# Optimization experiments

Hardware: AMD Instinct MI355X
Metric: run time of the kernel (lower is better)

## Reference

```python
import jax, jax.numpy as jnp
from jax import lax
import numpy as np

L, B, C, H, W = 2, 4, 256, 128, 128
D = C // 2            # complex feature dim per head (embed_dim // 2)
NH = 2                # hardcoded n_heads in ComplexTransformerEncoderLayer
KS, STRIDE, PAD = 9, 8, 4
SCALE = 32.0 ** -0.5  # n_head_channels ** -0.5 (hardcoded 32)

_PNAMES = ['wq','bq','wk','bk','wv','bv','off_dw_w','off_dw_b','off_ln_g','off_ln_b',
           'off_pw_w','fc1_wr','fc1_wi','fc1_br','fc1_bi','fc2_wr','fc2_wi','fc2_br',
           'fc2_bi','ln_grr','ln_gri','ln_gii','ln_br','ln_bi','rpe_table']


def _bilinear(img, grid):
    # img: (Cc, Hi, Wi); grid: (..., 2) with (x, y) in [-1, 1]
    # matches F.grid_sample(mode='bilinear', align_corners=True, padding_mode='zeros')
    Cc, Hi, Wi = img.shape
    x = (grid[..., 0] + 1.0) * 0.5 * (Wi - 1)
    y = (grid[..., 1] + 1.0) * 0.5 * (Hi - 1)
    x0 = jnp.floor(x); y0 = jnp.floor(y)
    x1 = x0 + 1.0; y1 = y0 + 1.0
    wx1 = x - x0; wx0 = 1.0 - wx1
    wy1 = y - y0; wy0 = 1.0 - wy1

    def tap(yy, xx, wgt):
        valid = (xx >= 0) & (xx <= Wi - 1) & (yy >= 0) & (yy <= Hi - 1)
        xi = jnp.clip(xx, 0, Wi - 1).astype(jnp.int32)
        yi = jnp.clip(yy, 0, Hi - 1).astype(jnp.int32)
        v = img[:, yi, xi]                      # (Cc, *grid_shape)
        return v * (wgt * valid.astype(img.dtype))[None]

    return (tap(y0, x0, wy0 * wx0) + tap(y0, x1, wy0 * wx1)
            + tap(y1, x0, wy1 * wx0) + tap(y1, x1, wy1 * wx1))

_grid_sample = jax.vmap(_bilinear)


def _cln(a, b, gam, eps=1e-20):
    # complex layer-norm via 2x2 covariance whitening over the last (feature) dim
    grr, gri, gii, br, bi = gam
    a = a - a.mean(-1, keepdims=True)
    b = b - b.mean(-1, keepdims=True)
    vrr = (a * a).mean(-1, keepdims=True) + eps
    vii = (b * b).mean(-1, keepdims=True) + eps
    vri = (a * b).mean(-1, keepdims=True)
    s = jnp.sqrt(vrr * vii - vri * vri)
    t = jnp.sqrt(vrr + vii + 2.0 * s)
    inv = 1.0 / (s * t)
    wrr = (vii + s) * inv; wii = (vrr + s) * inv; wri = -vri * inv
    na = wrr * a + wri * b
    nb = wri * a + wii * b
    return grr * na + gri * nb + br, gri * na + gii * nb + bi


def _layer(xa, xb, p):
    res_a = xa.reshape(B * NH, D, H * W).transpose(2, 0, 1)  # (HW, B*NH, D)
    res_b = xb.reshape(B * NH, D, H * W).transpose(2, 0, 1)

    def proj(x, w, bias):  # 1x1 conv
        return jnp.einsum('bchw,oc->bohw', x, w) + bias[None, :, None, None]

    qa = proj(xa, p['wq'], p['bq'])
    qb = proj(xb, p['wq'], p['bq'])

    def conv_offset(q):
        y = lax.conv_general_dilated(q, p['off_dw_w'], (STRIDE, STRIDE),
                                     ((PAD, PAD), (PAD, PAD)),
                                     feature_group_count=C,
                                     dimension_numbers=('NCHW', 'OIHW', 'NCHW'))
        y = y + p['off_dw_b'][None, :, None, None]
        m = y.mean(1, keepdims=True)
        v = ((y - m) ** 2).mean(1, keepdims=True)
        y = (y - m) * lax.rsqrt(v + 1e-5)
        y = y * p['off_ln_g'][None, :, None, None] + p['off_ln_b'][None, :, None, None]
        y = jax.nn.gelu(y, approximate=False)
        return jnp.einsum('bchw,pc->bhwp', y, p['off_pw_w'])  # (B, Hk, Wk, 2) in (y, x)

    off_a = conv_offset(qa)
    off_b = conv_offset(qb)
    Hk, Wk = off_a.shape[1], off_a.shape[2]
    ns = Hk * Wk

    ry = jnp.linspace(0.5, Hk - 0.5, Hk) / (Hk - 1.0) * 2.0 - 1.0
    rx = jnp.linspace(0.5, Wk - 0.5, Wk) / (Wk - 1.0) * 2.0 - 1.0
    ref = jnp.stack(jnp.meshgrid(ry, rx, indexing='ij'), -1)  # (Hk, Wk, 2) (y, x)
    pos_a = off_a + ref
    pos_b = off_b + ref

    xs_a = _grid_sample(xa, pos_a[..., ::-1])  # (B, C, Hk, Wk)
    xs_b = _grid_sample(xb, pos_b[..., ::-1])

    ka = proj(xs_a, p['wk'], p['bk']).reshape(B * NH, D, ns)
    va = proj(xs_a, p['wv'], p['bv']).reshape(B * NH, D, ns)
    kb = proj(xs_b, p['wk'], p['bk']).reshape(B * NH, D, ns)
    vb = proj(xs_b, p['wv'], p['bv']).reshape(B * NH, D, ns)
    qa_ = qa.reshape(B * NH, D, H * W)
    qb_ = qb.reshape(B * NH, D, H * W)

    # Re( q * conj(k) ); imaginary part is discarded by attn.real in the original
    attn = SCALE * (jnp.einsum('bcm,bcn->bmn', qa_, ka)
                    + jnp.einsum('bcm,bcn->bmn', qb_, kb))

    # deformable RPE bias; only the real (a) branch survives attn.real
    gy = jnp.arange(H, dtype=xa.dtype) / (H - 1.0) * 2.0 - 1.0
    gx = jnp.arange(W, dtype=xa.dtype) / (W - 1.0) * 2.0 - 1.0
    qg = jnp.stack(jnp.meshgrid(gy, gx, indexing='ij'), -1).reshape(H * W, 2)
    disp_a = (qg[None, :, None, :] - pos_a.reshape(B, ns, 2)[:, None, :, :]) * 0.5
    rpe = jnp.broadcast_to(p['rpe_table'][None], (B, NH, 2 * H - 1, 2 * W - 1))
    bias_a = _grid_sample(rpe, disp_a[..., ::-1]).reshape(B * NH, H * W, ns)

    attn = jax.nn.softmax(attn + bias_a, axis=2)
    oa = jnp.einsum('bmn,bcn->bcm', attn, va).transpose(2, 0, 1)  # (HW, B*NH, D)
    ob = jnp.einsum('bmn,bcn->bcm', attn, vb).transpose(2, 0, 1)

    oa, ob = _cln(oa, ob, (p['ln_grr'][0], p['ln_gri'][0], p['ln_gii'][0],
                           p['ln_br'][0], p['ln_bi'][0]))
    xa2 = res_a + oa
    xb2 = res_b + ob

    def clinear(a, b, wr, wi, br, bi):
        ya = a @ wr.T - b @ wi.T + br
        yb = a @ wi.T + b @ wr.T + bi
        return ya, yb

    ha, hb = clinear(xa2, xb2, p['fc1_wr'], p['fc1_wi'], p['fc1_br'], p['fc1_bi'])
    ha = jax.nn.relu(ha); hb = jax.nn.relu(hb)
    ha, hb = clinear(ha, hb, p['fc2_wr'], p['fc2_wi'], p['fc2_br'], p['fc2_bi'])
    ha, hb = _cln(ha, hb, (p['ln_grr'][1], p['ln_gri'][1], p['ln_gii'][1],
                           p['ln_br'][1], p['ln_bi'][1]))
    xa3 = xa2 + ha
    xb3 = xb2 + hb
    return (xa3.transpose(1, 2, 0).reshape(B, C, H, W),
            xb3.transpose(1, 2, 0).reshape(B, C, H, W))


def _forward(x_A, x_B, stacked):
    for l in range(L):
        p = {n: stacked[n][l] for n in _PNAMES}
        x_A, x_B = _layer(x_A, x_B, p)
    return x_A, x_B


def setup_inputs():
    key = jax.random.key(0)
    ks = jax.random.split(key, 12)
    f32 = jnp.float32
    return {
        'x_A': jax.random.normal(ks[0], (B, C, H, W), f32),
        'x_B': jax.random.normal(ks[1], (B, C, H, W), f32),
        'wq': jax.random.normal(ks[2], (L, C, C), f32) / np.float32(np.sqrt(C)),
        'bq': jnp.zeros((L, C), f32),
        'wk': jax.random.normal(ks[3], (L, C, C), f32) / np.float32(np.sqrt(C)),
        'bk': jnp.zeros((L, C), f32),
        'wv': jax.random.normal(ks[4], (L, C, C), f32) / np.float32(np.sqrt(C)),
        'bv': jnp.zeros((L, C), f32),
        'off_dw_w': jax.random.normal(ks[5], (L, C, 1, KS, KS), f32) * 0.05,
        'off_dw_b': jnp.zeros((L, C), f32),
        'off_ln_g': jnp.ones((L, C), f32),
        'off_ln_b': jnp.zeros((L, C), f32),
        'off_pw_w': jax.random.normal(ks[6], (L, 2, C), f32) * 0.01,
        'fc1_wr': jax.random.normal(ks[7], (L, D, D), f32) / np.float32(np.sqrt(D)),
        'fc1_wi': jax.random.normal(ks[8], (L, D, D), f32) / np.float32(np.sqrt(D)),
        'fc1_br': jnp.zeros((L, D), f32),
        'fc1_bi': jnp.zeros((L, D), f32),
        'fc2_wr': jax.random.normal(ks[9], (L, D, D), f32) / np.float32(np.sqrt(D)),
        'fc2_wi': jax.random.normal(ks[10], (L, D, D), f32) / np.float32(np.sqrt(D)),
        'fc2_br': jnp.zeros((L, D), f32),
        'fc2_bi': jnp.zeros((L, D), f32),
        'ln_grr': jnp.full((L, 2, D), 1.0 / np.sqrt(2.0), f32),
        'ln_gri': jnp.zeros((L, 2, D), f32),
        'ln_gii': jnp.full((L, 2, D), 1.0 / np.sqrt(2.0), f32),
        'ln_br': jnp.zeros((L, 2, D), f32),
        'ln_bi': jnp.zeros((L, 2, D), f32),
        # original forward creates rpe_table as fresh zeros each call
        'rpe_table': jnp.zeros((L, NH, 2 * H - 1, 2 * W - 1), f32),
    }


def reference(x_A, x_B, wq, bq, wk, bk, wv, bv, off_dw_w, off_dw_b, off_ln_g, off_ln_b,
              off_pw_w, fc1_wr, fc1_wi, fc1_br, fc1_bi, fc2_wr, fc2_wi, fc2_br, fc2_bi,
              ln_grr, ln_gri, ln_gii, ln_br, ln_bi, rpe_table):
    vals = (wq, bq, wk, bk, wv, bv, off_dw_w, off_dw_b, off_ln_g, off_ln_b, off_pw_w,
            fc1_wr, fc1_wi, fc1_br, fc1_bi, fc2_wr, fc2_wi, fc2_br, fc2_bi,
            ln_grr, ln_gri, ln_gii, ln_br, ln_bi, rpe_table)
    stacked = {n: v for n, v in zip(_PNAMES, vals)}
    return _forward(x_A, x_B, stacked)
```

## Files before the change

### kernel.cpp

```cpp
#include <hip/hip_runtime.h>
#include <math.h>

#define DEVFN static __device__ __forceinline__

constexpr int LAYERS = 2;
constexpr int Bz = 4;
constexpr int Cc = 256;
constexpr int Hh = 128;
constexpr int Ww = 128;
constexpr int Dd = 128;
constexpr int NHh = 2;
constexpr int BHt = Bz * NHh;
constexpr int Mt  = Hh * Ww;
constexpr int HK = 16, WK = 16;
constexpr int NSs = HK * WK;
constexpr int STR = 8, PADc = 4;
constexpr int RPH = 2*Hh - 1, RPW = 2*Ww - 1;
constexpr float SCALE_F = 0.17677669529663687f;

typedef __attribute__((ext_vector_type(8))) short  bf16x8;
typedef __attribute__((ext_vector_type(4))) float  f32x4;

DEVFN float wsum64(float v) {
    #pragma unroll
// ... 146 lines not shown
            const uint4 w1 = *(const uint4*)(bufc + ((a0 + 16) ^ sw));
            bf16x8 wh, wl; unpack8(w0, w1, wh, wl);
            acc[nt] = __builtin_amdgcn_mfma_f32_16x16x32_bf16(wh, xh[cs], acc[nt], 0, 0, 0);
            acc[nt] = __builtin_amdgcn_mfma_f32_16x16x32_bf16(wh, xl[cs], acc[nt], 0, 0, 0);
            acc[nt] = __builtin_amdgcn_mfma_f32_16x16x32_bf16(wl, xh[cs], acc[nt], 0, 0, 0);
        }
        __syncthreads();
    }

    #pragma unroll
    for (int nt = 0; nt < 16; nt++) {
        #pragma unroll
        for (int r = 0; r < 4; r++) {
            const int o = nt*16 + g*4 + r;
            ot[o*68 + w*16 + l15] = acc[nt][r] + bias[o];
        }
    }
    __syncthreads();
    #pragma unroll
    for (int it = 0; it < 16; it++) {
        const int idx = it*256 + tid;
        const int o = idx >> 4, mq = idx & 15;
        const float4 v = *(const float4*)&ot[o*68 + mq*4];
        *(float4*)(Out + ((size_t)b*Cc + o)*Mt + m0 + mq*4) = v;
    }
}

__global__ __launch_bounds__(256)
void k_dwconv(const float* __restrict__ Q, const float* __restrict__ Wdw,
              const float* __restrict__ Bdw, float* __restrict__ Y)
{
    const int c = blockIdx.x, b = blockIdx.y;
    __shared__ float wsmem[81];
    const int tid = threadIdx.x;
    if (tid < 81) wsmem[tid] = Wdw[c*81 + tid];
    __syncthreads();
    const int i = tid >> 4, j = tid & 15;
    const float* Qc = Q + ((size_t)b*Cc + c)*Mt;
    float acc = Bdw[c];
    const int ybase = i*STR - PADc, xbase = j*STR - PADc;
    #pragma unroll
    for (int u = 0; u < 9; u++) {
        const int y = ybase + u;
        if (y < 0 || y >= Hh) continue;
        #pragma unroll
        for (int v = 0; v < 9; v++) {
            const int x = xbase + v;
            if (x < 0 || x >= Ww) continue;
            acc += wsmem[u*9+v] * Qc[y*Ww + x];
        }
    }
    Y[((size_t)b*Cc + c)*NSs + i*WK + j] = acc;
}

DEVFN float block_reduce(float v, float* red, int tid)
{
    red[tid] = v; __syncthreads();
    #pragma unroll
    for (int s2 = 128; s2 > 0; s2 >>= 1) {
        if (tid < s2) red[tid] += red[tid + s2];
        __syncthreads();
    }
    const float r = red[0];
    __syncthreads();
    return r;
}

__global__ __launch_bounds__(256)
void k_lnpw(const float* __restrict__ Y, const float* __restrict__ G,
            const float* __restrict__ Bt, const float* __restrict__ PW,
            float* __restrict__ Pos)
{
    __shared__ float red[256];
    const int ij = blockIdx.x, b = blockIdx.y;
    const int tid = threadIdx.x;
    const float y = Y[((size_t)b*Cc + tid)*NSs + ij];
    const float m = block_reduce(y, red, tid) * (1.f/256.f);
    const float d = y - m;
    const float v = block_reduce(d*d, red, tid) * (1.f/256.f);
    const float g = d * rsqrtf(v + 1e-5f) * G[tid] + Bt[tid];
    const float ge = 0.5f * g * (1.f + erff(g * 0.70710678118654752f));
    const float off0 = block_reduce(ge * PW[tid], red, tid);
    const float off1 = block_reduce(ge * PW[Cc + tid], red, tid);
    if (tid == 0) {
        const int i = ij >> 4, j = ij & 15;
        const float refy = ((float)i + 0.5f) * (2.f/15.f) - 1.f;
        const float refx = ((float)j + 0.5f) * (2.f/15.f) - 1.f;
        Pos[((size_t)b*NSs + ij)*2 + 0] = off0 + refy;
        Pos[((size_t)b*NSs + ij)*2 + 1] = off1 + refx;
    }
}

__global__ __launch_bounds__(256)
void k_gsample(const float* __restrict__ X, const float* __restrict__ Pos,
               float* __restrict__ Xs)
{
    const int c = blockIdx.x, b = blockIdx.y, s = threadIdx.x;
    const float py = Pos[((size_t)b*NSs + s)*2 + 0];
    const float px = Pos[((size_t)b*NSs + s)*2 + 1];
    const float x = (px + 1.f) * 0.5f * (float)(Ww - 1);
    const float y = (py + 1.f) * 0.5f * (float)(Hh - 1);
    const float x0 = floorf(x), y0 = floorf(y);
    const float wx1 = x - x0, wx0 = 1.f - wx1;
    const float wy1 = y - y0, wy0 = 1.f - wy1;
    const float* Xc = X + ((size_t)b*Cc + c)*Mt;
    float acc = 0.f;
    #pragma unroll
    for (int t = 0; t < 4; t++) {
        const float xx = x0 + (float)(t & 1);
        const float yy = y0 + (float)(t >> 1);
        float w = ((t & 1) ? wx1 : wx0) * ((t >> 1) ? wy1 : wy0);
        const bool valid = (xx >= 0.f) && (xx <= (float)(Ww-1)) &&
                           (yy >= 0.f) && (yy <= (float)(Hh-1));
        const int xi = (int)fminf(fmaxf(xx, 0.f), (float)(Ww-1));
        const int yi = (int)fminf(fmaxf(yy, 0.f), (float)(Hh-1));
        acc += (valid ? w : 0.f) * Xc[yi*Ww + xi];
    }
    Xs[((size_t)b*Cc + c)*NSs + s] = acc;
}

__global__ __launch_bounds__(256)
void k_qsplit(const float* __restrict__ Qa, const float* __restrict__ Qb,
              uint* __restrict__ Qs)
{
    __shared__ float tile[64][65];
    const int tid = threadIdx.x;
    const int m0 = blockIdx.x * 64;
    const int bh = blockIdx.y;
    const int b = bh >> 1, h = bh & 1;
    for (int ccblk = 0; ccblk < 4; ccblk++) {
        #pragma unroll
        for (int i = 0; i < 4; i++) {
            const int idx = i*256 + tid;
            const int ccl = idx >> 4, mq = idx & 15;
            const int cc2 = ccblk*64 + ccl;
            const float* src = (cc2 >> 7) ? Qb : Qa;
            *(float4*)&tile[ccl][mq*4] =
                *(const float4*)(src + ((size_t)b*Cc + h*Dd + (cc2 & 127))*Mt + m0 + mq*4);
        }
        __syncthreads();
        #pragma unroll
        for (int i = 0; i < 16; i++) {
            const int idx = i*256 + tid;
            const int ml = idx >> 6, ccl = idx & 63;
            ushort hi, lo; split2(tile[ccl][ml], hi, lo);
            Qs[((size_t)bh*Mt + m0 + ml)*256 + ccblk*64 + ccl] = ((uint)hi << 16) | lo;
        }
        __syncthreads();
    }
}

__global__ __launch_bounds__(256)
void k_ksplit(const float* __restrict__ Ka, const float* __restrict__ Kb,
              uint* __restrict__ Ktp)
{
    __shared__ float tile[64][65];
    const int tid = threadIdx.x;
    const int n0 = blockIdx.x * 64;
    const int bh = blockIdx.y;
    const int b = bh >> 1, h = bh & 1;
    for (int ccblk = 0; ccblk < 4; ccblk++) {
        #pragma unroll
        for (int i = 0; i < 16; i++) {
            const int idx = i*256 + tid;
            const int ccl = idx >> 6, nl = idx & 63;
            const int cc2 = ccblk*64 + ccl;
            const float* src = (cc2 >> 7) ? Kb : Ka;
            tile[ccl][nl] = src[((size_t)b*Cc + h*Dd + (cc2 & 127))*NSs + n0 + nl];
        }
        __syncthreads();
        #pragma unroll
        for (int i = 0; i < 16; i++) {
            const int idx = i*256 + tid;
            const int nl = idx >> 6, ccl = idx & 63;
            ushort hi, lo; split2(tile[ccl][nl], hi, lo);
            Ktp[((size_t)bh*NSs + n0 + nl)*256 + ccblk*64 + ccl] = ((uint)hi << 16) | lo;
        }
        __syncthreads();
    }
}

__global__ __launch_bounds__(256)
void k_vsplit(const float* __restrict__ Va, const float* __restrict__ Vb,
              uint* __restrict__ Vsp)
{
    const size_t e = (size_t)blockIdx.x*256 + threadIdx.x;
    const int n  = (int)(e & 255);
    const int j  = (int)((e >> 8) & 255);
    const int bh = (int)(e >> 16);
    const int b = bh >> 1, h = bh & 1;
    const float* src = (j >> 7) ? Vb : Va;
    const float v = src[((size_t)b*Cc + h*Dd + (j & 127))*NSs + n];
    ushort hi, lo; split2(v, hi, lo);
    Vsp[e] = ((uint)hi << 16) | lo;
}

__global__ __launch_bounds__(256)
void k_wsplit4(const float* __restrict__ W0, const float* __restrict__ W1,
               const float* __restrict__ W2, const float* __restrict__ W3,
               uint* __restrict__ Wp)
{
    const int mat = blockIdx.y;
    const float* W = (mat == 0) ? W0 : (mat == 1) ? W1 : (mat == 2) ? W2 : W3;
    const int i = blockIdx.x*256 + threadIdx.x;
    ushort hi, lo; split2(W[i], hi, lo);
    Wp[(size_t)mat*Dd*Dd + i] = ((uint)hi << 16) | lo;
}

__global__ __launch_bounds__(256)
void k_wsplit1(const float* __restrict__ W, uint* __restrict__ Wp)
{
    const int i = blockIdx.x*256 + threadIdx.x;
    ushort hi, lo; split2(W[i], hi, lo);
    Wp[i] = ((uint)hi << 16) | lo;
}

__global__ __launch_bounds__(256, 2)
void k_attn_mfma(const uint* __restrict__ Qs, const uint* __restrict__ Ktp,
                 const uint* __restrict__ Vsp,
                 const float* __restrict__ Pos, const float* __restrict__ Rpe,
                 float* __restrict__ Oa, float* __restrict__ Ob)
{
    constexpr int GS = 66;
    __shared__ ushort Gt[NSs * GS];
    __shared__ float fxs[NSs];
    __shared__ __align__(16) uint kvbuf[2][4096];
    const int tid = threadIdx.x;
    const int m0 = blockIdx.x * 64;
    const int bh = blockIdx.y;
    const int b = bh >> 1, h = bh & 1;
    const int j0 = m0 & 127;
    const int iq = m0 >> 7;
    const float* Rh = Rpe + (size_t)h * RPH * RPW;

    {
        const int n = tid;
        const float py = Pos[((size_t)b*NSs + n)*2 + 0];
        const float px = Pos[((size_t)b*NSs + n)*2 + 1];
        const float xf = (float)j0 + 63.5f - 63.5f*px;
        const float yf = (float)iq + 63.5f - 63.5f*py;
        const float xbf = floorf(xf), ybf = floorf(yf);
        const float fx = xf - xbf, fy = yf - ybf;
        fxs[n] = fx;
        const int yb = (int)ybf;
        const float wy0 = (1.f - fy) * ((yb   >= 0 && yb   <= RPH-1) ? 1.f : 0.f);
        const float wy1 = fy         * ((yb+1 >= 0 && yb+1 <= RPH-1) ? 1.f : 0.f);
        const int y0c = yb   < 0 ? 0 : (yb   > RPH-1 ? RPH-1 : yb);
        const int y1c = yb+1 < 0 ? 0 : (yb+1 > RPH-1 ? RPH-1 : yb+1);
        const float* r0 = Rh + (size_t)y0c * RPW;
        const float* r1 = Rh + (size_t)y1c * RPW;
        const int xb = (int)xbf;
        #pragma unroll 4
        for (int t = 0; t <= 64; t++) {
            const int xi = xb + t;
            const int xc = xi < 0 ? 0 : (xi > RPW-1 ? RPW-1 : xi);
            const float v = wy0*r0[xc] + wy1*r1[xc];
            Gt[n*GS + t] = f2bf((xi >= 0 && xi <= RPW-1) ? v : 0.f);
        }
    }

    const int w = tid >> 6, l = tid & 63;
    const int l15 = l & 15, g = l >> 4;
    const int mcol = m0 + w*16 + l15;

    const uint* kbase = Ktp + (size_t)bh * 65536;
    const uint* vbase = Vsp + (size_t)bh * 65536;
    char* const kv0 = (char*)&kvbuf[0][0];
    char* const kv1 = (char*)&kvbuf[1][0];
    auto stage = [&](int p, const uint* chunk) {
        char* dst = p ? kv1 : kv0;
        #pragma unroll
        for (int r = 0; r < 4; r++) {
            const int idx = r*1024 + tid*4;
            const uint4 v = *(const uint4*)(chunk + idx);
            const int byte = idx << 2;
            const int swz = ((byte >> 10) & 7) << 4;
            *(uint4*)(dst + (byte ^ swz)) = v;
        }
    };

    bf16x8 qh[8], ql[8];
    {
        const uint* qp = Qs + ((size_t)bh*Mt + mcol)*256 + g*8;
        #pragma unroll
        for (int cs = 0; cs < 8; cs++) {
            const uint4 q0 = *(const uint4*)(qp + cs*32);
            const uint4 q1 = *(const uint4*)(qp + cs*32 + 4);
            unpack8(q0, q1, qh[cs], ql[cs]);
        }
    }

    f32x4 acc[16];
    #pragma unroll
    for (int nt = 0; nt < 16; nt++) acc[nt] = (f32x4){0.f, 0.f, 0.f, 0.f};

    const int rowb = l15 << 10;
    const int sw = (l15 & 7) << 4;

    stage(0, kbase);
    __syncthreads();
    #pragma unroll
    for (int nt = 0; nt < 16; nt++) {
        if (nt < 15) stage((nt + 1) & 1, kbase + (nt + 1)*4096);
        const char* bufc = (nt & 1) ? kv1 : kv0;
        #pragma unroll
        for (int cs = 0; cs < 8; cs++) {
            const int a0 = rowb + cs*128 + g*32;
            const uint4 k0 = *(const uint4*)(bufc + (a0 ^ sw));
            const uint4 k1 = *(const uint4*)(bufc + ((a0 + 16) ^ sw));
            bf16x8 kh, kl; unpack8(k0, k1, kh, kl);
            acc[nt] = __builtin_amdgcn_mfma_f32_16x16x32_bf16(kh, qh[cs], acc[nt], 0, 0, 0);
            acc[nt] = __builtin_amdgcn_mfma_f32_16x16x32_bf16(kh, ql[cs], acc[nt], 0, 0, 0);
            acc[nt] = __builtin_amdgcn_mfma_f32_16x16x32_bf16(kl, qh[cs], acc[nt], 0, 0, 0);
        }
        __syncthreads();
    }

    const int dm = w*16 + l15;
    float mx = -1e30f;
    #pragma unroll
    for (int nt = 0; nt < 16; nt++) {
        #pragma unroll
        for (int r = 0; r < 4; r++) {
            const int n = nt*16 + g*4 + r;
            const float g0 = bf2f(Gt[n*GS + dm]);
            const float g1 = bf2f(Gt[n*GS + dm + 1]);
            const float bias = g0 + fxs[n]*(g1 - g0);
            const float s = SCALE_F*acc[nt][r] + bias;
            acc[nt][r] = s;
            mx = fmaxf(mx, s);
        }
    }
    mx = fmaxf(mx, __shfl_xor(mx, 16, 64));
    mx = fmaxf(mx, __shfl_xor(mx, 32, 64));
    float sum = 0.f;
    #pragma unroll
    for (int nt = 0; nt < 16; nt++)
        #pragma unroll
        for (int r = 0; r < 4; r++) {
            const float e = __expf(acc[nt][r] - mx);
            acc[nt][r] = e;
            sum += e;
        }
    sum += __shfl_xor(sum, 16, 64);
    sum += __shfl_xor(sum, 32, 64);
    const float inv = 1.f / sum;

    uint hU0[16], hU1[16], lU0[16], lU1[16];
    #pragma unroll
    for (int nt = 0; nt < 16; nt++) {
        ushort ph_[4], pl_[4];
        #pragma unroll
        for (int r = 0; r < 4; r++) split2(acc[nt][r] * inv, ph_[r], pl_[r]);
        hU0[nt] = (uint)ph_[0] | ((uint)ph_[1] << 16);
        hU1[nt] = (uint)ph_[2] | ((uint)ph_[3] << 16);
        lU0[nt] = (uint)pl_[0] | ((uint)pl_[1] << 16);
        lU1[nt] = (uint)pl_[2] | ((uint)pl_[3] << 16);
    }

    const int srcA = (((2*g)     & 3) << 4) | l15;
    const int srcB = (((2*g + 1) & 3) << 4) | l15;
    const bool hi2 = (g >> 1) & 1;
    bf16x8 ph[8], pl[8];
    #pragma unroll
    for (int cs = 0; cs < 8; cs++) {
        uint A00 = shfu(hU0[2*cs], srcA), A01 = shfu(hU0[2*cs+1], srcA);
        uint A10 = shfu(hU1[2*cs], srcA), A11 = shfu(hU1[2*cs+1], srcA);
        uint B00 = shfu(hU0[2*cs], srcB), B01 = shfu(hU0[2*cs+1], srcB);
        uint B10 = shfu(hU1[2*cs], srcB), B11 = shfu(hU1[2*cs+1], srcB);
        ph[cs] = pack4(hi2 ? A01 : A00, hi2 ? A11 : A10,
                       hi2 ? B01 : B00, hi2 ? B11 : B10);
        A00 = shfu(lU0[2*cs], srcA); A01 = shfu(lU0[2*cs+1], srcA);
        A10 = shfu(lU1[2*cs], srcA); A11 = shfu(lU1[2*cs+1], srcA);
        B00 = shfu(lU0[2*cs], srcB); B01 = shfu(lU0[2*cs+1], srcB);
        B10 = shfu(lU1[2*cs], srcB); B11 = shfu(lU1[2*cs+1], srcB);
        pl[cs] = pack4(hi2 ? A01 : A00, hi2 ? A11 : A10,
                       hi2 ? B01 : B00, hi2 ? B11 : B10);
    }

    const size_t rowbase = ((size_t)bh*Mt + mcol)*Dd;
    stage(0, vbase);
    __syncthreads();
    for (int jt = 0; jt < 16; jt++) {
        if (jt < 15) stage((jt + 1) & 1, vbase + (jt + 1)*4096);
        const char* bufc = (jt & 1) ? kv1 : kv0;
        f32x4 a2 = (f32x4){0.f, 0.f, 0.f, 0.f};
        #pragma unroll
        for (int cs = 0; cs < 8; cs++) {
            const int a0 = rowb + cs*128 + g*32;
            const uint4 v0 = *(const uint4*)(bufc + (a0 ^ sw));
            const uint4 v1 = *(const uint4*)(bufc + ((a0 + 16) ^ sw));
            bf16x8 vh, vl; unpack8(v0, v1, vh, vl);
            a2 = __builtin_amdgcn_mfma_f32_16x16x32_bf16(vh, ph[cs], a2, 0, 0, 0);
            a2 = __builtin_amdgcn_mfma_f32_16x16x32_bf16(vh, pl[cs], a2, 0, 0, 0);
            a2 = __builtin_amdgcn_mfma_f32_16x16x32_bf16(vl, ph[cs], a2, 0, 0, 0);
        }
        const float4 o = make_float4(a2[0], a2[1], a2[2], a2[3]);
        const int jv0 = jt*16 + g*4;
        if (jt < 8) *(float4*)(Oa + rowbase + jv0) = o;
        else        *(float4*)(Ob + rowbase + jv0 - 128) = o;
        __syncthreads();
    }
}

__global__ __launch_bounds__(256)
void k_cln_attn(const float* __restrict__ Oa, const float* __restrict__ Ob,
                const float* __restrict__ Xa, const float* __restrict__ Xb,
                const float* __restrict__ Pgrr, const float* __restrict__ Pgri,
                const float* __restrict__ Pgii, const float* __restrict__ Pbr,
                const float* __restrict__ Pbi,
                float* __restrict__ X2a, float* __restrict__ X2b)
{
    __shared__ float ra[32][132];
    __shared__ float rb[32][132];
    const int tid = threadIdx.x;
    const int m0 = blockIdx.x * 32;
    const int bh = blockIdx.y;
    const int b = bh >> 1, h = bh & 1;
    {
        const float* Xpa = Xa + ((size_t)b*Cc + h*Dd)*Mt + m0;
        const float* Xpb = Xb + ((size_t)b*Cc + h*Dd)*Mt + m0;
        for (int idx = tid; idx < 1024; idx += 256) {
            const int c = idx >> 3, jq = idx & 7;
            float4 a4 = *(const float4*)(Xpa + (size_t)c*Mt + jq*4);
            float4 b4 = *(const float4*)(Xpb + (size_t)c*Mt + jq*4);
            ra[jq*4+0][c] = a4.x; ra[jq*4+1][c] = a4.y;
            ra[jq*4+2][c] = a4.z; ra[jq*4+3][c] = a4.w;
            rb[jq*4+0][c] = b4.x; rb[jq*4+1][c] = b4.y;
            rb[jq*4+2][c] = b4.z; rb[jq*4+3][c] = b4.w;
        }
    }
    __syncthreads();
    const int wave = tid >> 6, lane = tid & 63;
    const float grr0 = Pgrr[lane], grr1 = Pgrr[lane+64];
    const float gri0 = Pgri[lane], gri1 = Pgri[lane+64];
    const float gii0 = Pgii[lane], gii1 = Pgii[lane+64];
    const float br0  = Pbr[lane],  br1  = Pbr[lane+64];
    const float bi0  = Pbi[lane],  bi1  = Pbi[lane+64];
    for (int r = wave; r < 32; r += 4) {
        const size_t rowoff = ((size_t)bh*Mt + m0 + r)*Dd;
        float a0 = Oa[rowoff + lane], a1 = Oa[rowoff + lane + 64];
        float c0 = Ob[rowoff + lane], c1 = Ob[rowoff + lane + 64];
        const float ma = wsum64(a0 + a1) * (1.f/128.f);
        const float mb = wsum64(c0 + c1) * (1.f/128.f);
        a0 -= ma; a1 -= ma; c0 -= mb; c1 -= mb;
        const float vrr = wsum64(a0*a0 + a1*a1) * (1.f/128.f) + 1e-20f;
        const float vii = wsum64(c0*c0 + c1*c1) * (1.f/128.f) + 1e-20f;
        const float vri = wsum64(a0*c0 + a1*c1) * (1.f/128.f);
        const float s = sqrtf(fmaxf(vrr*vii - vri*vri, 0.f));
        const float t = sqrtf(vrr + vii + 2.f*s);
        const float inv = 1.f / (s*t);
        const float wrr = (vii + s)*inv, wii = (vrr + s)*inv, wri = -vri*inv;
        const float na0 = wrr*a0 + wri*c0, nb0 = wri*a0 + wii*c0;
        const float na1 = wrr*a1 + wri*c1, nb1 = wri*a1 + wii*c1;
        X2a[rowoff + lane]      = ra[r][lane]    + grr0*na0 + gri0*nb0 + br0;
        X2a[rowoff + lane + 64] = ra[r][lane+64] + grr1*na1 + gri1*nb1 + br1;
        X2b[rowoff + lane]      = rb[r][lane]    + gri0*na0 + gii0*nb0 + bi0;
        X2b[rowoff + lane + 64] = rb[r][lane+64] + gri1*na1 + gii1*nb1 + bi1;
    }
}

__global__ __launch_bounds__(256)
void k_ffn_mfma(const float* __restrict__ A, const float* __restrict__ Bm,
                const uint* __restrict__ Wrp, const uint* __restrict__ Wip,
                const float* __restrict__ br, const float* __restrict__ bi,
                float* __restrict__ Ha, float* __restrict__ Hb, int relu)
{
    const int tid = threadIdx.x;
    const size_t r0 = (size_t)blockIdx.x * 64;
    const int w = tid >> 6, l = tid & 63;
    const int l15 = l & 15, g = l >> 4;
    const size_t row = r0 + (size_t)w*16 + l15;

    f32x4 accr[8], acci[8];
    #pragma unroll
    for (int nt = 0; nt < 8; nt++) {
        accr[nt] = (f32x4){0.f, 0.f, 0.f, 0.f};
        acci[nt] = (f32x4){0.f, 0.f, 0.f, 0.f};
    }

    const float* ap = A  + row*Dd + g*8;
    const float* bp = Bm + row*Dd + g*8;
    const uint*  wr = Wrp + l15*Dd + g*8;
    const uint*  wi = Wip + l15*Dd + g*8;

    #pragma unroll
    for (int cs = 0; cs < 4; cs++) {
        const float4 a0 = *(const float4*)(ap + cs*32);
        const float4 a1 = *(const float4*)(ap + cs*32 + 4);
        const float4 b0 = *(const float4*)(bp + cs*32);
        const float4 b1 = *(const float4*)(bp + cs*32 + 4);
        const float av[8] = {a0.x,a0.y,a0.z,a0.w,a1.x,a1.y,a1.z,a1.w};
        const float bv[8] = {b0.x,b0.y,b0.z,b0.w,b1.x,b1.y,b1.z,b1.w};
        bf16x8 ah, al, bh_, bl_, nh, nl;
        #pragma unroll
        for (int j = 0; j < 8; j++) {
            ushort h1, l1; split2(av[j], h1, l1);
            ah[j] = (short)h1; al[j] = (short)l1;
            split2(bv[j], h1, l1);
            bh_[j] = (short)h1; bl_[j] = (short)l1;
            nh[j] = (short)(h1 ^ 0x8000);
            nl[j] = (short)(l1 ^ 0x8000);
        }
        #pragma unroll
        for (int nt = 0; nt < 8; nt++) {
            const uint* wrp2 = wr + nt*2048 + cs*32;
            const uint* wip2 = wi + nt*2048 + cs*32;
            const uint4 r0v = *(const uint4*)(wrp2);
            const uint4 r1v = *(const uint4*)(wrp2 + 4);
            const uint4 i0v = *(const uint4*)(wip2);
            const uint4 i1v = *(const uint4*)(wip2 + 4);
            bf16x8 wrh, wrl, wih, wil;
            unpack8(r0v, r1v, wrh, wrl);
            unpack8(i0v, i1v, wih, wil);
            accr[nt] = __builtin_amdgcn_mfma_f32_16x16x32_bf16(wrh, ah, accr[nt], 0, 0, 0);
            accr[nt] = __builtin_amdgcn_mfma_f32_16x16x32_bf16(wrh, al, accr[nt], 0, 0, 0);
            accr[nt] = __builtin_amdgcn_mfma_f32_16x16x32_bf16(wrl, ah, accr[nt], 0, 0, 0);
            accr[nt] = __builtin_amdgcn_mfma_f32_16x16x32_bf16(wih, nh, accr[nt], 0, 0, 0);
            accr[nt] = __builtin_amdgcn_mfma_f32_16x16x32_bf16(wih, nl, accr[nt], 0, 0, 0);
            accr[nt] = __builtin_amdgcn_mfma_f32_16x16x32_bf16(wil, nh, accr[nt], 0, 0, 0);
            acci[nt] = __builtin_amdgcn_mfma_f32_16x16x32_bf16(wih, ah, acci[nt], 0, 0, 0);
            acci[nt] = __builtin_amdgcn_mfma_f32_16x16x32_bf16(wih, al, acci[nt], 0, 0, 0);
            acci[nt] = __builtin_amdgcn_mfma_f32_16x16x32_bf16(wil, ah, acci[nt], 0, 0, 0);
            acci[nt] = __builtin_amdgcn_mfma_f32_16x16x32_bf16(wrh, bh_, acci[nt], 0, 0, 0);
            acci[nt] = __builtin_amdgcn_mfma_f32_16x16x32_bf16(wrh, bl_, acci[nt], 0, 0, 0);
            acci[nt] = __builtin_amdgcn_mfma_f32_16x16x32_bf16(wrl, bh_, acci[nt], 0, 0, 0);
        }
    }

    #pragma unroll
    for (int nt = 0; nt < 8; nt++) {
        const int n0 = nt*16 + g*4;
        const float4 vbr = *(const float4*)(br + n0);
        const float4 vbi = *(const float4*)(bi + n0);
        const float brv[4] = {vbr.x, vbr.y, vbr.z, vbr.w};
        const float biv[4] = {vbi.x, vbi.y, vbi.z, vbi.w};
        float4 orv, oiv;
        float* po = &orv.x; float* pj = &oiv.x;
        #pragma unroll
        for (int r = 0; r < 4; r++) {
            float hr = accr[nt][r] + brv[r];
            float hi = acci[nt][r] + biv[r];
            if (relu) { hr = fmaxf(hr, 0.f); hi = fmaxf(hi, 0.f); }
            po[r] = hr; pj[r] = hi;
        }
        *(float4*)(Ha + row*Dd + n0) = orv;
        *(float4*)(Hb + row*Dd + n0) = oiv;
    }
}

__global__ __launch_bounds__(256)
void k_cln_ffn(const float* __restrict__ Ha2, const float* __restrict__ Hb2,
               const float* __restrict__ X2a, const float* __restrict__ X2b,
               const float* __restrict__ Pgrr, const float* __restrict__ Pgri,
               const float* __restrict__ Pgii, const float* __restrict__ Pbr,
               const float* __restrict__ Pbi,
               float* __restrict__ OutA, float* __restrict__ OutB)
{
    __shared__ float oA[128][36];
    __shared__ float oB[128][36];
    const int tid = threadIdx.x;
    const int m0 = blockIdx.x * 32;
    const int bh = blockIdx.y;
    const int b = bh >> 1, h = bh & 1;
    const int wave = tid >> 6, lane = tid & 63;
    const float grr0 = Pgrr[lane], grr1 = Pgrr[lane+64];
    const float gri0 = Pgri[lane], gri1 = Pgri[lane+64];
    const float gii0 = Pgii[lane], gii1 = Pgii[lane+64];
    const float br0  = Pbr[lane],  br1  = Pbr[lane+64];
    const float bi0  = Pbi[lane],  bi1  = Pbi[lane+64];
    for (int r = wave; r < 32; r += 4) {
        const size_t rowoff = ((size_t)bh*Mt + m0 + r)*Dd;
        float a0 = Ha2[rowoff + lane], a1 = Ha2[rowoff + lane + 64];
        float c0 = Hb2[rowoff + lane], c1 = Hb2[rowoff + lane + 64];
        const float ma = wsum64(a0 + a1) * (1.f/128.f);
        const float mb = wsum64(c0 + c1) * (1.f/128.f);
        a0 -= ma; a1 -= ma; c0 -= mb; c1 -= mb;
        const float vrr = wsum64(a0*a0 + a1*a1) * (1.f/128.f) + 1e-20f;
        const float vii = wsum64(c0*c0 + c1*c1) * (1.f/128.f) + 1e-20f;
        const float vri = wsum64(a0*c0 + a1*c1) * (1.f/128.f);
        const float s = sqrtf(fmaxf(vrr*vii - vri*vri, 0.f));
        const float t = sqrtf(vrr + vii + 2.f*s);
        const float inv = 1.f / (s*t);
        const float wrr = (vii + s)*inv, wii = (vrr + s)*inv, wri = -vri*inv;
        const float na0 = wrr*a0 + wri*c0, nb0 = wri*a0 + wii*c0;
        const float na1 = wrr*a1 + wri*c1, nb1 = wri*a1 + wii*c1;
        oA[lane][r]    = X2a[rowoff + lane]      + grr0*na0 + gri0*nb0 + br0;
        oA[lane+64][r] = X2a[rowoff + lane + 64] + grr1*na1 + gri1*nb1 + br1;
        oB[lane][r]    = X2b[rowoff + lane]      + gri0*na0 + gii0*nb0 + bi0;
        oB[lane+64][r] = X2b[rowoff + lane + 64] + gri1*na1 + gii1*nb1 + bi1;
    }
    __syncthreads();
    const size_t obase = ((size_t)b*Cc + h*Dd)*Mt + m0;
    for (int idx = tid; idx < 1024; idx += 256) {
        const int c = idx >> 3, jq = idx & 7;
        *(float4*)(OutA + obase + (size_t)c*Mt + jq*4) = *(const float4*)&oA[c][jq*4];
        *(float4*)(OutB + obase + (size_t)c*Mt + jq*4) = *(const float4*)&oB[c][jq*4];
    }
}

extern "C" void kernel_launch(void* const* d_in, const int* in_sizes, int n_in,
                              void* d_out, int out_size, void* d_ws, size_t ws_size,
                              hipStream_t stream)
{
    const float* xA0 = (const float*)d_in[0];
    const float* xB0 = (const float*)d_in[1];
    const float* wq  = (const float*)d_in[2];
    const float* bq  = (const float*)d_in[3];
    const float* wk  = (const float*)d_in[4];
    const float* bk  = (const float*)d_in[5];
    const float* wv  = (const float*)d_in[6];
    const float* bv  = (const float*)d_in[7];
    const float* dww = (const float*)d_in[8];
    const float* dwb = (const float*)d_in[9];
    const float* lng = (const float*)d_in[10];
    const float* lnb = (const float*)d_in[11];
    const float* pw  = (const float*)d_in[12];
    const float* f1wr = (const float*)d_in[13];
    const float* f1wi = (const float*)d_in[14];
    const float* f1br = (const float*)d_in[15];
    const float* f1bi = (const float*)d_in[16];
    const float* f2wr = (const float*)d_in[17];
    const float* f2wi = (const float*)d_in[18];
    const float* f2br = (const float*)d_in[19];
    const float* f2bi = (const float*)d_in[20];
    const float* lgrr = (const float*)d_in[21];
    const float* lgri = (const float*)d_in[22];
    const float* lgii = (const float*)d_in[23];
    const float* lbr  = (const float*)d_in[24];
    const float* lbi  = (const float*)d_in[25];
    const float* rpe  = (const float*)d_in[26];

    float* ws = (float*)d_ws;
    const size_t NB = (size_t)Bz * Cc * Mt;
    const size_t SC = (size_t)Bz * Cc * NSs;
    float* Pa  = ws;        float* Pb  = Pa  + NB;
    float* Ra  = Pb  + NB;  float* Rb  = Ra  + NB;
    float* Ya  = Rb  + NB;  float* Yb  = Ya  + SC;
    float* XsA = Yb  + SC;  float* XsB = XsA + SC;
    float* Kab = XsB + SC;  float* Kbb = Kab + SC;
    float* Vab = Kbb + SC;  float* Vbb = Vab + SC;
    float* Sp0 = Vbb + SC;  float* Sp1 = Sp0 + SC;
    float* PosA = Sp1 + SC; float* PosB = PosA + (size_t)Bz*NSs*2;
    float* Wpf  = PosB + (size_t)Bz*NSs*2;

    uint* Qs  = (uint*)Ra;
    uint* Ktp = (uint*)Sp0;
    uint* Vsp = (uint*)Ya;
    uint* Wp  = (uint*)Wpf;
    uint* Wqp = Wp + (size_t)4*Dd*Dd;

    float* outAf = (float*)d_out;
    float* outBf = outAf + NB;

    for (int l = 0; l < LAYERS; l++) {
        const float* pwq = wq + (size_t)l*Cc*Cc;
        const float* pbq = bq + (size_t)l*Cc;
        const float* pwk = wk + (size_t)l*Cc*Cc;
        const float* pbk = bk + (size_t)l*Cc;
        const float* pwv = wv + (size_t)l*Cc*Cc;
        const float* pbv = bv + (size_t)l*Cc;
        const float* pdww = dww + (size_t)l*Cc*81;
        const float* pdwb = dwb + (size_t)l*Cc;
        const float* plng = lng + (size_t)l*Cc;
        const float* plnb = lnb + (size_t)l*Cc;
        const float* ppw  = pw  + (size_t)l*2*Cc;
        const float* p1wr = f1wr + (size_t)l*Dd*Dd;
        const float* p1wi = f1wi + (size_t)l*Dd*Dd;
        const float* p1br = f1br + (size_t)l*Dd;
        const float* p1bi = f1bi + (size_t)l*Dd;
        const float* p2wr = f2wr + (size_t)l*Dd*Dd;
        const float* p2wi = f2wi + (size_t)l*Dd*Dd;
        const float* p2br = f2br + (size_t)l*Dd;
        const float* p2bi = f2bi + (size_t)l*Dd;
        const float* g0rr = lgrr + (size_t)(l*2+0)*Dd;
        const float* g0ri = lgri + (size_t)(l*2+0)*Dd;
        const float* g0ii = lgii + (size_t)(l*2+0)*Dd;
        const float* g0br = lbr  + (size_t)(l*2+0)*Dd;
        const float* g0bi = lbi  + (size_t)(l*2+0)*Dd;
        const float* g1rr = lgrr + (size_t)(l*2+1)*Dd;
        const float* g1ri = lgri + (size_t)(l*2+1)*Dd;
        const float* g1ii = lgii + (size_t)(l*2+1)*Dd;
        const float* g1br = lbr  + (size_t)(l*2+1)*Dd;
        const float* g1bi = lbi  + (size_t)(l*2+1)*Dd;
        const float* prpe = rpe + (size_t)l*NHh*RPH*RPW;

        const float* inA = l ? outAf : xA0;
        const float* inB = l ? outBf : xB0;

        dim3 gW(64, 4);
        k_wsplit4<<<gW, 256, 0, stream>>>(p1wr, p1wi, p2wr, p2wi, Wp);
        k_wsplit1<<<256, 256, 0, stream>>>(pwq, Wqp);

        dim3 gQs(Mt/64, BHt);
        k_qsplit<<<gQs, 256, 0, stream>>>(inA, inB, Qs);

        dim3 gPQ(Mt/64, Bz);
        k_projq_mfma<<<gPQ, 256, 0, stream>>>(Qs, Wqp, pbq, Pa, 0);
        k_projq_mfma<<<gPQ, 256, 0, stream>>>(Qs, Wqp, pbq, Pb, 1);

        dim3 gD(Cc, Bz);
        k_dwconv<<<gD, 256, 0, stream>>>(Pa, pdww, pdwb, Ya);
        k_dwconv<<<gD, 256, 0, stream>>>(Pb, pdww, pdwb, Yb);

        dim3 gL(NSs, Bz);
        k_lnpw<<<gL, 256, 0, stream>>>(Ya, plng, plnb, ppw, PosA);
        k_lnpw<<<gL, 256, 0, stream>>>(Yb, plng, plnb, ppw, PosB);

        dim3 gS(Cc, Bz);
        k_gsample<<<gS, 256, 0, stream>>>(inA, PosA, XsA);
        k_gsample<<<gS, 256, 0, stream>>>(inB, PosB, XsB);

        dim3 gKV(NSs/64, Cc/64, Bz);
        k_proj<<<gKV, 256, 0, stream>>>(XsA, pwk, pbk, Kab, NSs);
        k_proj<<<gKV, 256, 0, stream>>>(XsB, pwk, pbk, Kbb, NSs);
        k_proj<<<gKV, 256, 0, stream>>>(XsA, pwv, pbv, Vab, NSs);
        k_proj<<<gKV, 256, 0, stream>>>(XsB, pwv, pbv, Vbb, NSs);

        dim3 gKs(NSs/64, BHt);
        k_ksplit<<<gKs, 256, 0, stream>>>(Kab, Kbb, Ktp);
        k_vsplit<<<2048, 256, 0, stream>>>(Vab, Vbb, Vsp);
        k_qsplit<<<gQs, 256, 0, stream>>>(Pa, Pb, Qs);

        dim3 gA(Mt/64, BHt);
        k_attn_mfma<<<gA, 256, 0, stream>>>(Qs, Ktp, Vsp, PosA, prpe, Pa, Pb);

        dim3 gC(Mt/32, BHt);
        k_cln_attn<<<gC, 256, 0, stream>>>(Pa, Pb, inA, inB,
                                           g0rr, g0ri, g0ii, g0br, g0bi, Ra, Rb);

        dim3 gF((unsigned)((size_t)BHt*Mt/64));
        k_ffn_mfma<<<gF, 256, 0, stream>>>(Ra, Rb, Wp, Wp + (size_t)Dd*Dd,
                                           p1br, p1bi, Pa, Pb, 1);
        k_ffn_mfma<<<gF, 256, 0, stream>>>(Pa, Pb, Wp + (size_t)2*Dd*Dd,
                                           Wp + (size_t)3*Dd*Dd,
                                           p2br, p2bi, Pa, Pb, 0);

        k_cln_ffn<<<gC, 256, 0, stream>>>(Pa, Pb, Ra, Rb,
                                          g1rr, g1ri, g1ii, g1br, g1bi, outAf, outBf);
    }
    (void)in_sizes; (void)n_in; (void)out_size; (void)ws_size;
}
```

Measured before the change: 2.558 ms.

## Split K/V bf16 hi/lo into planar arrays and stage FFN weights through LDS

The packed (hi<<16|lo) uint layout for K and V becomes two planar bf16 arrays. The attention kernel can then load bf16x8 MFMA operands straight from LDS without unpack shuffles. The FFN kernel now splits its activations up front and double-buffers weight tiles through swizzled shared memory instead of reading weights from global memory per lane. This trades extra LDS use and per-tile barriers in the FFN for fewer VALU unpack ops and less redundant global weight traffic.

```diff
diff --git a/kernel.cpp b/kernel.cpp
--- a/kernel.cpp
+++ b/kernel.cpp
@@ -322,7 +322,7 @@
 
 __global__ __launch_bounds__(256)
 void k_ksplit(const float* __restrict__ Ka, const float* __restrict__ Kb,
-              uint* __restrict__ Ktp)
+              ushort* __restrict__ KtpH, ushort* __restrict__ KtpL)
 {
     __shared__ float tile[64][65];
     const int tid = threadIdx.x;
@@ -340,11 +340,16 @@
         }
         __syncthreads();
         #pragma unroll
-        for (int i = 0; i < 16; i++) {
+        for (int i = 0; i < 8; i++) {
             const int idx = i*256 + tid;
-            const int nl = idx >> 6, ccl = idx & 63;
-            ushort hi, lo; split2(tile[ccl][nl], hi, lo);
-            Ktp[((size_t)bh*NSs + n0 + nl)*256 + ccblk*64 + ccl] = ((uint)hi << 16) | lo;
+            const int nl = idx >> 5, cp = idx & 31;
+            const int ccl = cp*2;
+            ushort h0, l0, h1, l1;
+            split2(tile[ccl][nl],     h0, l0);
+            split2(tile[ccl + 1][nl], h1, l1);
+            const size_t o = ((size_t)bh*NSs + n0 + nl)*256 + ccblk*64 + ccl;
+            *(uint*)&KtpH[o] = (uint)h0 | ((uint)h1 << 16);
+            *(uint*)&KtpL[o] = (uint)l0 | ((uint)l1 << 16);
         }
         __syncthreads();
     }
@@ -352,17 +357,20 @@
 
 __global__ __launch_bounds__(256)
 void k_vsplit(const float* __restrict__ Va, const float* __restrict__ Vb,
-              uint* __restrict__ Vsp)
-{
-    const size_t e = (size_t)blockIdx.x*256 + threadIdx.x;
+              ushort* __restrict__ VsH, ushort* __restrict__ VsL)
+{
+    const size_t e = ((size_t)blockIdx.x*256 + threadIdx.x) * 2;
     const int n  = (int)(e & 255);
     const int j  = (int)((e >> 8) & 255);
     const int bh = (int)(e >> 16);
     const int b = bh >> 1, h = bh & 1;
     const float* src = (j >> 7) ? Vb : Va;
-    const float v = src[((size_t)b*Cc + h*Dd + (j & 127))*NSs + n];
-    ushort hi, lo; split2(v, hi, lo);
-    Vsp[e] = ((uint)hi << 16) | lo;
+    const float* p = src + ((size_t)b*Cc + h*Dd + (j & 127))*NSs + n;
+    ushort h0, l0, h1, l1;
+    split2(p[0], h0, l0);
+    split2(p[1], h1, l1);
+    *(uint*)&VsH[e] = (uint)h0 | ((uint)h1 << 16);
+    *(uint*)&VsL[e] = (uint)l0 | ((uint)l1 << 16);
 }
 
 __global__ __launch_bounds__(256)
@@ -386,15 +394,16 @@
 }
 
 __global__ __launch_bounds__(256, 2)
-void k_attn_mfma(const uint* __restrict__ Qs, const uint* __restrict__ Ktp,
-                 const uint* __restrict__ Vsp,
+void k_attn_mfma(const uint* __restrict__ Qs,
+                 const ushort* __restrict__ KtpH, const ushort* __restrict__ KtpL,
+                 const ushort* __restrict__ VsH,  const ushort* __restrict__ VsL,
                  const float* __restrict__ Pos, const float* __restrict__ Rpe,
                  float* __restrict__ Oa, float* __restrict__ Ob)
 {
     constexpr int GS = 66;
     __shared__ ushort Gt[NSs * GS];
     __shared__ float fxs[NSs];
-    __shared__ __align__(16) uint kvbuf[2][4096];
+    __shared__ __align__(16) char kvbuf[2][16384];
     const int tid = threadIdx.x;
     const int m0 = blockIdx.x * 64;
     const int bh = blockIdx.y;
@@ -433,19 +442,22 @@
     const int l15 = l & 15, g = l >> 4;
     const int mcol = m0 + w*16 + l15;
 
-    const uint* kbase = Ktp + (size_t)bh * 65536;
-    const uint* vbase = Vsp + (size_t)bh * 65536;
-    char* const kv0 = (char*)&kvbuf[0][0];
-    char* const kv1 = (char*)&kvbuf[1][0];
-    auto stage = [&](int p, const uint* chunk) {
+    const ushort* kbaseH = KtpH + (size_t)bh * 65536;
+    const ushort* kbaseL = KtpL + (size_t)bh * 65536;
+    const ushort* vbaseH = VsH  + (size_t)bh * 65536;
+    const ushort* vbaseL = VsL  + (size_t)bh * 65536;
+    char* const kv0 = kvbuf[0];
+    char* const kv1 = kvbuf[1];
+    auto stage = [&](int p, const ushort* hs, const ushort* ls) {
         char* dst = p ? kv1 : kv0;
         #pragma unroll
-        for (int r = 0; r < 4; r++) {
-            const int idx = r*1024 + tid*4;
-            const uint4 v = *(const uint4*)(chunk + idx);
-            const int byte = idx << 2;
-            const int swz = ((byte >> 10) & 7) << 4;
-            *(uint4*)(dst + (byte ^ swz)) = v;
+        for (int r = 0; r < 2; r++) {
+            const int byte = r*4096 + tid*16;
+            const int swz = ((byte >> 9) & 7) << 4;
+            *(uint4*)(dst + (byte ^ swz)) =
+                *(const uint4*)((const char*)hs + byte);
+            *(uint4*)(dst + 8192 + (byte ^ swz)) =
+                *(const uint4*)((const char*)ls + byte);
         }
     };
 
@@ -464,21 +476,21 @@
     #pragma unroll
     for (int nt = 0; nt < 16; nt++) acc[nt] = (f32x4){0.f, 0.f, 0.f, 0.f};
 
-    const int rowb = l15 << 10;
+    const int rowb = l15 << 9;
     const int sw = (l15 & 7) << 4;
 
-    stage(0, kbase);
+    stage(0, kbaseH, kbaseL);
     __syncthreads();
     #pragma unroll
     for (int nt = 0; nt < 16; nt++) {
-        if (nt < 15) stage((nt + 1) & 1, kbase + (nt + 1)*4096);
+        if (nt < 15) stage((nt + 1) & 1,
+                           kbaseH + (nt + 1)*4096, kbaseL + (nt + 1)*4096);
         const char* bufc = (nt & 1) ? kv1 : kv0;
         #pragma unroll
         for (int cs = 0; cs < 8; cs++) {
-            const int a0 = rowb + cs*128 + g*32;
-            const uint4 k0 = *(const uint4*)(bufc + (a0 ^ sw));
-            const uint4 k1 = *(const uint4*)(bufc + ((a0 + 16) ^ sw));
-            bf16x8 kh, kl; unpack8(k0, k1, kh, kl);
+            const int a0 = rowb + cs*64 + g*16;
+            const bf16x8 kh = *(const bf16x8*)(bufc + (a0 ^ sw));
+            const bf16x8 kl = *(const bf16x8*)(bufc + 8192 + (a0 ^ sw));
             acc[nt] = __builtin_amdgcn_mfma_f32_16x16x32_bf16(kh, qh[cs], acc[nt], 0, 0, 0);
             acc[nt] = __builtin_amdgcn_mfma_f32_16x16x32_bf16(kh, ql[cs], acc[nt], 0, 0, 0);
             acc[nt] = __builtin_amdgcn_mfma_f32_16x16x32_bf16(kl, qh[cs], acc[nt], 0, 0, 0);
@@ -549,18 +561,18 @@
     }
 
     const size_t rowbase = ((size_t)bh*Mt + mcol)*Dd;
-    stage(0, vbase);
+    stage(0, vbaseH, vbaseL);
     __syncthreads();
     for (int jt = 0; jt < 16; jt++) {
-        if (jt < 15) stage((jt + 1) & 1, vbase + (jt + 1)*4096);
+        if (jt < 15) stage((jt + 1) & 1,
+                           vbaseH + (jt + 1)*4096, vbaseL + (jt + 1)*4096);
         const char* bufc = (jt & 1) ? kv1 : kv0;
         f32x4 a2 = (f32x4){0.f, 0.f, 0.f, 0.f};
         #pragma unroll
         for (int cs = 0; cs < 8; cs++) {
-            const int a0 = rowb + cs*128 + g*32;
-            const uint4 v0 = *(const uint4*)(bufc + (a0 ^ sw));
-            const uint4 v1 = *(const uint4*)(bufc + ((a0 + 16) ^ sw));
-            bf16x8 vh, vl; unpack8(v0, v1, vh, vl);
+            const int a0 = rowb + cs*64 + g*16;
+            const bf16x8 vh = *(const bf16x8*)(bufc + (a0 ^ sw));
+            const bf16x8 vl = *(const bf16x8*)(bufc + 8192 + (a0 ^ sw));
             a2 = __builtin_amdgcn_mfma_f32_16x16x32_bf16(vh, ph[cs], a2, 0, 0, 0);
             a2 = __builtin_amdgcn_mfma_f32_16x16x32_bf16(vh, pl[cs], a2, 0, 0, 0);
             a2 = __builtin_amdgcn_mfma_f32_16x16x32_bf16(vl, ph[cs], a2, 0, 0, 0);
@@ -636,12 +648,37 @@
                 const float* __restrict__ br, const float* __restrict__ bi,
                 float* __restrict__ Ha, float* __restrict__ Hb, int relu)
 {
+    __shared__ __align__(16) char wbuf[2][16384];
     const int tid = threadIdx.x;
     const size_t r0 = (size_t)blockIdx.x * 64;
     const int w = tid >> 6, l = tid & 63;
     const int l15 = l & 15, g = l >> 4;
     const size_t row = r0 + (size_t)w*16 + l15;
 
+    bf16x8 ah[4], al[4], bh_[4], bl_[4], nh[4], nl[4];
+    {
+        const float* ap = A  + row*Dd + g*8;
+        const float* bp = Bm + row*Dd + g*8;
+        #pragma unroll
+        for (int cs = 0; cs < 4; cs++) {
+            const float4 a0 = *(const float4*)(ap + cs*32);
+            const float4 a1 = *(const float4*)(ap + cs*32 + 4);
+            const float4 b0 = *(const float4*)(bp + cs*32);
+            const float4 b1 = *(const float4*)(bp + cs*32 + 4);
+            const float av[8] = {a0.x,a0.y,a0.z,a0.w,a1.x,a1.y,a1.z,a1.w};
+            const float bv[8] = {b0.x,b0.y,b0.z,b0.w,b1.x,b1.y,b1.z,b1.w};
+            #pragma unroll
+            for (int j = 0; j < 8; j++) {
+                ushort h1, l1; split2(av[j], h1, l1);
+                ah[cs][j] = (short)h1; al[cs][j] = (short)l1;
+                split2(bv[j], h1, l1);
+                bh_[cs][j] = (short)h1; bl_[cs][j] = (short)l1;
+                nh[cs][j] = (short)(h1 ^ 0x8000);
+                nl[cs][j] = (short)(l1 ^ 0x8000);
+            }
+        }
+    }
+
     f32x4 accr[8], acci[8];
     #pragma unroll
     for (int nt = 0; nt < 8; nt++) {
@@ -649,53 +686,50 @@
         acci[nt] = (f32x4){0.f, 0.f, 0.f, 0.f};
     }
 
-    const float* ap = A  + row*Dd + g*8;
-    const float* bp = Bm + row*Dd + g*8;
-    const uint*  wr = Wrp + l15*Dd + g*8;
-    const uint*  wi = Wip + l15*Dd + g*8;
-
-    #pragma unroll
-    for (int cs = 0; cs < 4; cs++) {
-        const float4 a0 = *(const float4*)(ap + cs*32);
-        const float4 a1 = *(const float4*)(ap + cs*32 + 4);
-        const float4 b0 = *(const float4*)(bp + cs*32);
-        const float4 b1 = *(const float4*)(bp + cs*32 + 4);
-        const float av[8] = {a0.x,a0.y,a0.z,a0.w,a1.x,a1.y,a1.z,a1.w};
-        const float bv[8] = {b0.x,b0.y,b0.z,b0.w,b1.x,b1.y,b1.z,b1.w};
-        bf16x8 ah, al, bh_, bl_, nh, nl;
-        #pragma unroll
-        for (int j = 0; j < 8; j++) {
-            ushort h1, l1; split2(av[j], h1, l1);
-            ah[j] = (short)h1; al[j] = (short)l1;
-            split2(bv[j], h1, l1);
-            bh_[j] = (short)h1; bl_[j] = (short)l1;
-            nh[j] = (short)(h1 ^ 0x8000);
-            nl[j] = (short)(l1 ^ 0x8000);
-        }
-        #pragma unroll
-        for (int nt = 0; nt < 8; nt++) {
-            const uint* wrp2 = wr + nt*2048 + cs*32;
-            const uint* wip2 = wi + nt*2048 + cs*32;
-            const uint4 r0v = *(const uint4*)(wrp2);
-            const uint4 r1v = *(const uint4*)(wrp2 + 4);
-            const uint4 i0v = *(const uint4*)(wip2);
-            const uint4 i1v = *(const uint4*)(wip2 + 4);
+    auto stage = [&](int p, const uint* wr_, const uint* wi_) {
+        char* dst = wbuf[p];
+        #pragma unroll
+        for (int r = 0; r < 2; r++) {
+            const int byte = r*4096 + tid*16;
+            const int swz = ((byte >> 9) & 7) << 4;
+            *(uint4*)(dst + (byte ^ swz)) =
+                *(const uint4*)((const char*)wr_ + byte);
+            *(uint4*)(dst + 8192 + (byte ^ swz)) =
+                *(const uint4*)((const char*)wi_ + byte);
+        }
+    };
+
+    const int sw = (l15 & 7) << 4;
+    stage(0, Wrp, Wip);
+    __syncthreads();
+    #pragma unroll
+    for (int nt = 0; nt < 8; nt++) {
+        if (nt < 7) stage((nt + 1) & 1, Wrp + (nt + 1)*2048, Wip + (nt + 1)*2048);
+        const char* bufc = wbuf[nt & 1];
+        #pragma unroll
+        for (int cs = 0; cs < 4; cs++) {
+            const int a0 = (l15 << 9) + cs*128 + g*32;
+            const uint4 r0v = *(const uint4*)(bufc + (a0 ^ sw));
+            const uint4 r1v = *(const uint4*)(bufc + ((a0 + 16) ^ sw));
+            const uint4 i0v = *(const uint4*)(bufc + 8192 + (a0 ^ sw));
+            const uint4 i1v = *(const uint4*)(bufc + 8192 + ((a0 + 16) ^ sw));
             bf16x8 wrh, wrl, wih, wil;
             unpack8(r0v, r1v, wrh, wrl);
             unpack8(i0v, i1v, wih, wil);
-            accr[nt] = __builtin_amdgcn_mfma_f32_16x16x32_bf16(wrh, ah, accr[nt], 0, 0, 0);
-            accr[nt] = __builtin_amdgcn_mfma_f32_16x16x32_bf16(wrh, al, accr[nt], 0, 0, 0);
-            accr[nt] = __builtin_amdgcn_mfma_f32_16x16x32_bf16(wrl, ah, accr[nt], 0, 0, 0);
-            accr[nt] = __builtin_amdgcn_mfma_f32_16x16x32_bf16(wih, nh, accr[nt], 0, 0, 0);
-            accr[nt] = __builtin_amdgcn_mfma_f32_16x16x32_bf16(wih, nl, accr[nt], 0, 0, 0);
-            accr[nt] = __builtin_amdgcn_mfma_f32_16x16x32_bf16(wil, nh, accr[nt], 0, 0, 0);
-            acci[nt] = __builtin_amdgcn_mfma_f32_16x16x32_bf16(wih, ah, acci[nt], 0, 0, 0);
-            acci[nt] = __builtin_amdgcn_mfma_f32_16x16x32_bf16(wih, al, acci[nt], 0, 0, 0);
-            acci[nt] = __builtin_amdgcn_mfma_f32_16x16x32_bf16(wil, ah, acci[nt], 0, 0, 0);
-            acci[nt] = __builtin_amdgcn_mfma_f32_16x16x32_bf16(wrh, bh_, acci[nt], 0, 0, 0);
-            acci[nt] = __builtin_amdgcn_mfma_f32_16x16x32_bf16(wrh, bl_, acci[nt], 0, 0, 0);
-            acci[nt] = __builtin_amdgcn_mfma_f32_16x16x32_bf16(wrl, bh_, acci[nt], 0, 0, 0);
-        }
+            accr[nt] = __builtin_amdgcn_mfma_f32_16x16x32_bf16(wrh, ah[cs],  accr[nt], 0, 0, 0);
+            accr[nt] = __builtin_amdgcn_mfma_f32_16x16x32_bf16(wrh, al[cs],  accr[nt], 0, 0, 0);
+            accr[nt] = __builtin_amdgcn_mfma_f32_16x16x32_bf16(wrl, ah[cs],  accr[nt], 0, 0, 0);
+            accr[nt] = __builtin_amdgcn_mfma_f32_16x16x32_bf16(wih, nh[cs],  accr[nt], 0, 0, 0);
+            accr[nt] = __builtin_amdgcn_mfma_f32_16x16x32_bf16(wih, nl[cs],  accr[nt], 0, 0, 0);
+            accr[nt] = __builtin_amdgcn_mfma_f32_16x16x32_bf16(wil, nh[cs],  accr[nt], 0, 0, 0);
+            acci[nt] = __builtin_amdgcn_mfma_f32_16x16x32_bf16(wih, ah[cs],  acci[nt], 0, 0, 0);
+            acci[nt] = __builtin_amdgcn_mfma_f32_16x16x32_bf16(wih, al[cs],  acci[nt], 0, 0, 0);
+            acci[nt] = __builtin_amdgcn_mfma_f32_16x16x32_bf16(wil, ah[cs],  acci[nt], 0, 0, 0);
+            acci[nt] = __builtin_amdgcn_mfma_f32_16x16x32_bf16(wrh, bh_[cs], acci[nt], 0, 0, 0);
+            acci[nt] = __builtin_amdgcn_mfma_f32_16x16x32_bf16(wrh, bl_[cs], acci[nt], 0, 0, 0);
+            acci[nt] = __builtin_amdgcn_mfma_f32_16x16x32_bf16(wrl, bh_[cs], acci[nt], 0, 0, 0);
+        }
+        __syncthreads();
     }
 
     #pragma unroll
@@ -814,11 +848,13 @@
     float* PosA = Sp1 + SC; float* PosB = PosA + (size_t)Bz*NSs*2;
     float* Wpf  = PosB + (size_t)Bz*NSs*2;
 
-    uint* Qs  = (uint*)Ra;
-    uint* Ktp = (uint*)Sp0;
-    uint* Vsp = (uint*)Ya;
-    uint* Wp  = (uint*)Wpf;
-    uint* Wqp = Wp + (size_t)4*Dd*Dd;
+    uint*   Qs   = (uint*)Ra;
+    ushort* KtpH = (ushort*)Sp0;
+    ushort* KtpL = (ushort*)Sp1;
+    ushort* VsH  = (ushort*)Ya;
+    ushort* VsL  = (ushort*)Yb;
+    uint*   Wp   = (uint*)Wpf;
+    uint*   Wqp  = Wp + (size_t)4*Dd*Dd;
 
     float* outAf = (float*)d_out;
     float* outBf = outAf + NB;
@@ -888,12 +924,13 @@
         k_proj<<<gKV, 256, 0, stream>>>(XsB, pwv, pbv, Vbb, NSs);
 
         dim3 gKs(NSs/64, BHt);
-        k_ksplit<<<gKs, 256, 0, stream>>>(Kab, Kbb, Ktp);
-        k_vsplit<<<2048, 256, 0, stream>>>(Vab, Vbb, Vsp);
+        k_ksplit<<<gKs, 256, 0, stream>>>(Kab, Kbb, KtpH, KtpL);
+        k_vsplit<<<1024, 256, 0, stream>>>(Vab, Vbb, VsH, VsL);
         k_qsplit<<<gQs, 256, 0, stream>>>(Pa, Pb, Qs);
 
         dim3 gA(Mt/64, BHt);
-        k_attn_mfma<<<gA, 256, 0, stream>>>(Qs, Ktp, Vsp, PosA, prpe, Pa, Pb);
+        k_attn_mfma<<<gA, 256, 0, stream>>>(Qs, KtpH, KtpL, VsH, VsL,
+                                            PosA, prpe, Pa, Pb);
 
         dim3 gC(Mt/32, BHt);
         k_cln_attn<<<gC, 256, 0, stream>>>(Pa, Pb, inA, inB,
```

Result: faster. 2.412 ms (-5.7%).
